# Performance work log

Measured on AMD Instinct MI355X. Metric: run time of the kernel, lower is better.

The kernel has to match this reference:

```python
import jax, jax.numpy as jnp
import numpy as np

B, L = 16, 4096          # trees per batch, leaves per tree (power of 2)
V, D, H, C = 50000, 256, 256, 2  # vocab, input_dim, hidden_dim, num_classes


def setup_inputs() -> dict:
    key = jax.random.key(0)
    ks = jax.random.split(key, 16)
    s = 0.02
    inp = {
        'leaf_ids': jax.random.randint(ks[0], (B, L), 0, V),
        'emb': jax.random.normal(ks[1], (V, D), jnp.float32) * s,
        'W_proj': jax.random.normal(ks[2], (D, H), jnp.float32) * s,
        'b_proj': jnp.zeros((H,), jnp.float32),
        'W_fl': jax.random.normal(ks[3], (2 * H, H), jnp.float32) * s,
        'b_fl': jnp.zeros((H,), jnp.float32),
        'W_fr': jax.random.normal(ks[4], (2 * H, H), jnp.float32) * s,
        'b_fr': jnp.zeros((H,), jnp.float32),
        'W_i': jax.random.normal(ks[5], (2 * H, H), jnp.float32) * s,
        'b_i': jnp.zeros((H,), jnp.float32),
        'W_o': jax.random.normal(ks[6], (2 * H, H), jnp.float32) * s,
        'b_o': jnp.zeros((H,), jnp.float32),
        'W_c': jax.random.normal(ks[7], (2 * H, H), jnp.float32) * s,
        'b_c': jnp.zeros((H,), jnp.float32),
        'W_cls': jax.random.normal(ks[8], (H, C), jnp.float32) * s,
        'b_cls': jnp.zeros((C,), jnp.float32),
    }
    return inp


def reference(leaf_ids, emb, W_proj, b_proj, W_fl, b_fl, W_fr, b_fr,
              W_i, b_i, W_o, b_o, W_c, b_c, W_cls, b_cls):
    # Leaf: hidden = Linear(embedding), cell = tanh(hidden)
    h = emb[leaf_ids] @ W_proj + b_proj          # [B, L, H]
    c = jnp.tanh(h)
    # Binary Tree-LSTM combine, one level at a time (log2(L) levels, static)
    while h.shape[1] > 1:
        hl, hr = h[:, 0::2], h[:, 1::2]          # [B, n/2, H]
        cl, cr = c[:, 0::2], c[:, 1::2]
        comb = jnp.concatenate([hl, hr], axis=-1)  # [B, n/2, 2H]
        fl = jax.nn.sigmoid(comb @ W_fl + b_fl)
        fr = jax.nn.sigmoid(comb @ W_fr + b_fr)
        ig = jax.nn.sigmoid(comb @ W_i + b_i)
        og = jax.nn.sigmoid(comb @ W_o + b_o)
        cc = jnp.tanh(comb @ W_c + b_c)
        c = fl * cl + fr * cr + ig * cc
        h = og * jnp.tanh(c)
    root_h = h[:, 0]                              # [B, H]
    return root_h @ W_cls + b_cls                 # [B, C] classification logits
```

## Files before the change

kernel.cpp:

```cpp
#include <hip/hip_runtime.h>
#include <hip/hip_bf16.h>

#define Hdim 256
#define Bdim 16
#define Lleaf 4096

typedef unsigned short u16;
typedef __attribute__((ext_vector_type(8))) short short8;
typedef __attribute__((ext_vector_type(4))) float f32x4;

__device__ __forceinline__ u16 f2bf(float x) {
    __hip_bfloat16 b = __float2bfloat16(x);
    return *(u16*)&b;
}
__device__ __forceinline__ float bf2f(u16 u) {
    __hip_bfloat16 b = *(__hip_bfloat16*)&u;
    return __bfloat162float(b);
}
__device__ __forceinline__ float fsig(float x) { return 1.0f / (1.0f + __expf(-x)); }
__device__ __forceinline__ float ftanh(float x) {
    float e = __expf(-2.0f * fabsf(x));
    float t = (1.0f - e) / (1.0f + e);
    return copysignf(t, x);
}

__device__ __forceinline__ void gload_lds16(const u16* gsrc, u16* ldsdst) {
    __builtin_amdgcn_global_load_lds(
        (const __attribute__((address_space(1))) unsigned int*)gsrc,
        (__attribute__((address_space(3))) unsigned int*)ldsdst, 16, 0, 0);
}

__global__ void pack_weights2(const float* __restrict__ Wfl, const float* __restrict__ Wfr,
                              const float* __restrict__ Wi,  const float* __restrict__ Wo,
                              const float* __restrict__ Wc,
                              u16* __restrict__ Wpk)
{
    int blk = blockIdx.x;
    int ng = blk >> 4, c = blk & 15;
    for (int e = threadIdx.x; e < 5120; e += 256) {
        int g = e >> 10, r = e & 1023;
        int t = r >> 9, s = r & 511;
        int lane = s >> 3, j = s & 7;
        int n = ng * 16 + (lane & 15);
        int k = c * 32 + (lane >> 4) * 8 + j;
        const float* W = (g == 0) ? Wfl : (g == 1) ? Wfr : (g == 2) ? Wi : (g == 3) ? Wo : Wc;
        float x = W[(size_t)k * Hdim + n];
        u16 hi = f2bf(x);
        u16 v = t ? f2bf(x - bf2f(hi)) : hi;
        Wpk[(size_t)blk * 5120 + e] = v;
    }
}

__global__ void pack_wp2(const float* __restrict__ Wp, u16* __restrict__ Wppk)
{
    int blk = blockIdx.x;
    int ng = blk >> 3, c = blk & 7;
    for (int e = threadIdx.x; e < 1024; e += 256) {
        int t = e >> 9, s = e & 511;
        int lane = s >> 3, j = s & 7;
        int n = ng * 16 + (lane & 15);
        int k = c * 32 + (lane >> 4) * 8 + j;
        float x = Wp[(size_t)k * Hdim + n];
        u16 hi = f2bf(x);
        u16 v = t ? f2bf(x - bf2f(hi)) : hi;
        Wppk[(size_t)blk * 1024 + e] = v;
    }
}

__global__ __launch_bounds__(256, 2) void leaf_mfma2(
    const int* __restrict__ ids, const float* __restrict__ emb,
    const u16* __restrict__ Wppk, const float* __restrict__ bp,
    u16* __restrict__ A0hi)
{
    int tid = threadIdx.x;
    int lane = tid & 63, w = tid >> 6;
    int l16 = lane & 15, quad = lane >> 4;
    int m0 = blockIdx.x * 128, ny = blockIdx.y;
    int n0 = ny * 64;

    const float* aptr[2];
#pragma unroll
    for (int mt = 0; mt < 2; mt++) {
        int m = m0 + w * 32 + mt * 16 + l16;
        aptr[mt] = emb + (size_t)ids[m] * 256 + quad * 8;
    }

    f32x4 acc[2][4];
    f32x4 zf = {0.f, 0.f, 0.f, 0.f};
#pragma unroll
    for (int i = 0; i < 2; i++)
#pragma unroll
        for (int j = 0; j < 4; j++) acc[i][j] = zf;

#pragma unroll 1
    for (int c = 0; c < 8; c++) {
        int k0 = c * 32;
        short8 bh[4], bl[4];
#pragma unroll
        for (int nt = 0; nt < 4; nt++) {
            const u16* pb = Wppk + (size_t)(((ny * 4 + nt) * 8 + c) * 2) * 512 + lane * 8;
            bh[nt] = *(const short8*)(pb);
            bl[nt] = *(const short8*)(pb + 512);
        }
        short8 ah[2], al[2];
#pragma unroll
        for (int mt = 0; mt < 2; mt++) {
            float4 a0 = *(const float4*)(aptr[mt] + k0);
            float4 a1 = *(const float4*)(aptr[mt] + k0 + 4);
            float fv[8] = {a0.x, a0.y, a0.z, a0.w, a1.x, a1.y, a1.z, a1.w};
#pragma unroll
            for (int e = 0; e < 8; e++) {
                u16 hv = f2bf(fv[e]);
                u16 lv = f2bf(fv[e] - bf2f(hv));
                ah[mt][e] = (short)hv;
                al[mt][e] = (short)lv;
            }
        }
#pragma unroll
        for (int nt = 0; nt < 4; nt++)
#pragma unroll
            for (int mt = 0; mt < 2; mt++) {
                acc[mt][nt] = __builtin_amdgcn_mfma_f32_16x16x32_bf16(ah[mt], bh[nt], acc[mt][nt], 0, 0, 0);
                acc[mt][nt] = __builtin_amdgcn_mfma_f32_16x16x32_bf16(al[mt], bh[nt], acc[mt][nt], 0, 0, 0);
                acc[mt][nt] = __builtin_amdgcn_mfma_f32_16x16x32_bf16(ah[mt], bl[nt], acc[mt][nt], 0, 0, 0);
            }
    }
#pragma unroll
    for (int mt = 0; mt < 2; mt++)
#pragma unroll
        for (int nt = 0; nt < 4; nt++)
#pragma unroll
            for (int r = 0; r < 4; r++) {
                int m = m0 + w * 32 + mt * 16 + quad * 4 + r;
                int n = n0 + nt * 16 + l16;
                float h = acc[mt][nt][r] + bp[n];
                A0hi[(size_t)(m >> 1) * 512 + (m & 1) * 256 + n] = f2bf(h);
            }
}

template <int LEAF, int WLO>
__global__ __launch_bounds__(256, 3) void level_big2(
    const u16* __restrict__ Ahi,
    const float* __restrict__ Cin,
    const u16* __restrict__ Wpk,
    const float* __restrict__ bfl, const float* __restrict__ bfr,
    const float* __restrict__ bi,  const float* __restrict__ bo,
    const float* __restrict__ bc,
    u16* __restrict__ Aohi, u16* __restrict__ Aolo, float* __restrict__ Cout,
    int M)
{
    int tid = threadIdx.x;
    int lane = tid & 63, w = tid >> 6;
    int l16 = lane & 15, quad = lane >> 4;
    int m0 = blockIdx.x * 64, n0 = blockIdx.y * 64;
    int ng = blockIdx.y * 4 + w;

    __shared__ u16 Abuf[2][8 * 512];

    const u16* asrc[2];
#pragma unroll
    for (int i = 0; i < 2; i++) {
        int fj = w * 2 + i;
        int s = fj >> 2, mf = fj & 3;
        int row = min(m0 + mf * 16 + l16, M - 1);
        asrc[i] = Ahi + (size_t)row * 512 + quad * 8 + s * 32;
    }
    const u16* pb = Wpk + (size_t)ng * 16 * 5120 + lane * 8;

    f32x4 acc[5][4];
    f32x4 zf = {0.f, 0.f, 0.f, 0.f};
#pragma unroll
    for (int g = 0; g < 5; g++)
#pragma unroll
        for (int mf = 0; mf < 4; mf++) acc[g][mf] = zf;

#pragma unroll
    for (int i = 0; i < 2; i++)
        gload_lds16(asrc[i], &Abuf[0][(w * 2 + i) * 512]);

#pragma unroll 1
    for (int c = 0; c < 8; c++) {
        __syncthreads();
        if (c < 7) {
#pragma unroll
            for (int i = 0; i < 2; i++)
                gload_lds16(asrc[i] + (c + 1) * 64, &Abuf[(c + 1) & 1][(w * 2 + i) * 512]);
        }
        const u16* ab = &Abuf[c & 1][0];
#pragma unroll
        for (int s = 0; s < 2; s++) {
            int c32 = c * 2 + s;
            short8 bh[5];
#pragma unroll
            for (int g = 0; g < 5; g++)
                bh[g] = *(const short8*)(pb + (size_t)(c32 * 10 + g * 2) * 512);
#pragma unroll
            for (int mf = 0; mf < 4; mf++) {
                short8 ah = *(const short8*)&ab[(s * 4 + mf) * 512 + lane * 8];
#pragma unroll
                for (int g = 0; g < 5; g++)
                    acc[g][mf] = __builtin_amdgcn_mfma_f32_16x16x32_bf16(ah, bh[g], acc[g][mf], 0, 0, 0);
            }
        }
    }

    int n = n0 + w * 16 + l16;
#pragma unroll
    for (int mf = 0; mf < 4; mf++)
#pragma unroll
        for (int r = 0; r < 4; r++) {
            int m = m0 + mf * 16 + quad * 4 + r;
            if (m >= M) continue;
            float fl = fsig(acc[0][mf][r] + bfl[n]);
            float fr = fsig(acc[1][mf][r] + bfr[n]);
            float ig = fsig(acc[2][mf][r] + bi[n]);
            float og = fsig(acc[3][mf][r] + bo[n]);
            float cc = ftanh(acc[4][mf][r] + bc[n]);
            float cl, cr;
            if (LEAF) {
                cl = ftanh(bf2f(Ahi[(size_t)m * 512 + n]));
                cr = ftanh(bf2f(Ahi[(size_t)m * 512 + 256 + n]));
            } else {
                cl = Cin[(size_t)(2 * m) * 256 + n];
                cr = Cin[(size_t)(2 * m + 1) * 256 + n];
            }
            float cn = fl * cl + fr * cr + ig * cc;
            Cout[(size_t)m * 256 + n] = cn;
            float h = og * ftanh(cn);
            u16 hh = f2bf(h);
            size_t ai = (size_t)(m >> 1) * 512 + (m & 1) * 256 + n;
            Aohi[ai] = hh;
            if (WLO) Aolo[ai] = f2bf(h - bf2f(hh));
        }
}

__global__ __launch_bounds__(256, 4) void level_small(
    const u16* __restrict__ Ahi, const u16* __restrict__ Alo,
    const float* __restrict__ Cin,
    const u16* __restrict__ Wpk,
    const float* __restrict__ bfl, const float* __restrict__ bfr,
    const float* __restrict__ bi,  const float* __restrict__ bo,
    const float* __restrict__ bc,
    u16* __restrict__ Aohi, u16* __restrict__ Aolo, float* __restrict__ Cout,
    int M)
{
    int tid = threadIdx.x;
    int lane = tid & 63, w = tid >> 6;
    int l16 = lane & 15, quad = lane >> 4;
    int mb = blockIdx.x * 16;
    int ng = blockIdx.y;

    const u16* pah = Ahi + (size_t)(mb + l16) * 512 + quad * 8;
    const u16* pal = Alo + (size_t)(mb + l16) * 512 + quad * 8;
    const u16* pb  = Wpk + (size_t)ng * 16 * 5120 + lane * 8;

    f32x4 acc[5];
    f32x4 zf = {0.f, 0.f, 0.f, 0.f};
#pragma unroll
    for (int g = 0; g < 5; g++) acc[g] = zf;

#pragma unroll
    for (int i = 0; i < 4; i++) {
        int c = w * 4 + i;
        short8 ah = *(const short8*)(pah + c * 32);
        short8 al = *(const short8*)(pal + c * 32);
#pragma unroll
        for (int g = 0; g < 5; g++) {
            short8 bh = *(const short8*)(pb + (size_t)(c * 10 + g * 2) * 512);
            short8 bl = *(const short8*)(pb + (size_t)(c * 10 + g * 2 + 1) * 512);
            acc[g] = __builtin_amdgcn_mfma_f32_16x16x32_bf16(ah, bh, acc[g], 0, 0, 0);
            acc[g] = __builtin_amdgcn_mfma_f32_16x16x32_bf16(al, bh, acc[g], 0, 0, 0);
            acc[g] = __builtin_amdgcn_mfma_f32_16x16x32_bf16(ah, bl, acc[g], 0, 0, 0);
        }
    }

    __shared__ float red[4][5][256];
#pragma unroll
    for (int g = 0; g < 5; g++)
#pragma unroll
        for (int r = 0; r < 4; r++)
            red[w][g][(quad * 4 + r) * 16 + l16] = acc[g][r];
    __syncthreads();

    int m = mb + (tid >> 4);
    int n = ng * 16 + (tid & 15);
    if (m < M) {
        float z[5];
#pragma unroll
        for (int g = 0; g < 5; g++)
            z[g] = red[0][g][tid] + red[1][g][tid] + red[2][g][tid] + red[3][g][tid];
        float fl = fsig(z[0] + bfl[n]);
        float fr = fsig(z[1] + bfr[n]);
        float ig = fsig(z[2] + bi[n]);
        float og = fsig(z[3] + bo[n]);
        float cc = ftanh(z[4] + bc[n]);
        float cl = Cin[(size_t)(2 * m) * 256 + n];
        float cr = Cin[(size_t)(2 * m + 1) * 256 + n];
        float cn = fl * cl + fr * cr + ig * cc;
        Cout[(size_t)m * 256 + n] = cn;
        float h = og * ftanh(cn);
        u16 hh = f2bf(h);
        u16 hl = f2bf(h - bf2f(hh));
        size_t ai = (size_t)(m >> 1) * 512 + (m & 1) * 256 + n;
        Aohi[ai] = hh;
        Aolo[ai] = hl;
    }
}

__global__ void classifier_bf(const u16* __restrict__ Ahi, const u16* __restrict__ Alo,
                              const float* __restrict__ Wcls, const float* __restrict__ bcls,
                              float* __restrict__ out)
{
    int t = threadIdx.x;
    if (t < Bdim * 2) {
        int b = t >> 1, cls = t & 1;
        float s = bcls[cls];
        for (int n = 0; n < Hdim; n++) {
            size_t ai = (size_t)(b >> 1) * 512 + (b & 1) * 256 + n;
            float h = bf2f(Ahi[ai]) + bf2f(Alo[ai]);
            s += h * Wcls[(size_t)n * 2 + cls];
        }
        out[t] = s;
    }
}

extern "C" void kernel_launch(void* const* d_in, const int* in_sizes, int n_in,
                              void* d_out, int out_size, void* d_ws, size_t ws_size,
                              hipStream_t stream) {
    const int*   ids  = (const int*)d_in[0];
    const float* emb  = (const float*)d_in[1];
    const float* Wp   = (const float*)d_in[2];
    const float* bp   = (const float*)d_in[3];
    const float* Wfl  = (const float*)d_in[4];
    const float* bfl  = (const float*)d_in[5];
    const float* Wfr  = (const float*)d_in[6];
    const float* bfr  = (const float*)d_in[7];
    const float* Wi   = (const float*)d_in[8];
    const float* bi   = (const float*)d_in[9];
    const float* Wo   = (const float*)d_in[10];
    const float* bo   = (const float*)d_in[11];
    const float* Wc   = (const float*)d_in[12];
    const float* bc   = (const float*)d_in[13];
    const float* Wcls = (const float*)d_in[14];
    const float* bcls = (const float*)d_in[15];

    u16* Wpk  = (u16*)d_ws;
    u16* Wppk = Wpk + (size_t)256 * 5120;
    unsigned char* base = (unsigned char*)d_ws + (4u << 20);
    unsigned char* R1 = base;
    unsigned char* R2 = base + 33554432;

    pack_weights2<<<256, 256, 0, stream>>>(Wfl, Wfr, Wi, Wo, Wc, Wpk);
    pack_wp2<<<128, 256, 0, stream>>>(Wp, Wppk);

    int M0 = Bdim * Lleaf;
    leaf_mfma2<<<dim3(M0 / 128, 4), 256, 0, stream>>>(ids, emb, Wppk, bp, (u16*)R1);

    const u16* Ain_hi = (const u16*)R1;
    const u16* Ain_lo = nullptr;
    const float* Cin = nullptr;

    int lev = 1;
    for (int M = 32768; M >= 16; M >>= 1, lev++) {
        unsigned char* ob = (lev & 1) ? R2 : R1;
        u16* Aohi = (u16*)ob;
        u16* Aolo = Aohi + (size_t)M * 256;
        float* Cout = (float*)(Aohi + (size_t)M * 512);
        if (lev == 1) {
            level_big2<1, 0><<<dim3(M / 64, 4), 256, 0, stream>>>(Ain_hi, nullptr, Wpk,
                                                                  bfl, bfr, bi, bo, bc, Aohi, Aolo, Cout, M);
        } else if (M > 4096) {
            level_big2<0, 0><<<dim3(M / 64, 4), 256, 0, stream>>>(Ain_hi, Cin, Wpk,
                                                                  bfl, bfr, bi, bo, bc, Aohi, Aolo, Cout, M);
        } else if (M == 4096) {
            level_big2<0, 1><<<dim3(M / 64, 4), 256, 0, stream>>>(Ain_hi, Cin, Wpk,
                                                                  bfl, bfr, bi, bo, bc, Aohi, Aolo, Cout, M);
        } else {
            level_small<<<dim3(M / 16, 16), 256, 0, stream>>>(Ain_hi, Ain_lo, Cin, Wpk,
                                                              bfl, bfr, bi, bo, bc, Aohi, Aolo, Cout, M);
        }
        Ain_hi = Aohi; Ain_lo = Aolo; Cin = Cout;
    }

    classifier_bf<<<1, 64, 0, stream>>>(Ain_hi, Ain_lo, Wcls, bcls, (float*)d_out);
}
```

Before: 395.1 us.

## Fuse last five tree levels into one per-tree kernel and drop leaf lo-split

Replaces the per-level launches for the bottom five tree levels (M=256 down to 16) with one tree_bottom kernel, one block per tree, that keeps hidden and cell state in shared memory across levels. Launch overhead and global round-trips for the tiny tail levels go away. Also drops the low-half bf16 split of the activations in the leaf projection GEMM, removing one MFMA of three. That lowers precision of leaf hidden states, and the fused kernel runs on only 16 blocks, so those five levels are serialized within each block.

New measurement: 582.8 us. 1.48x slower.

```diff
diff --git a/kernel.cpp b/kernel.cpp
--- a/kernel.cpp
+++ b/kernel.cpp
@@ -102,26 +102,20 @@
             bh[nt] = *(const short8*)(pb);
             bl[nt] = *(const short8*)(pb + 512);
         }
-        short8 ah[2], al[2];
+        short8 ah[2];
 #pragma unroll
         for (int mt = 0; mt < 2; mt++) {
             float4 a0 = *(const float4*)(aptr[mt] + k0);
             float4 a1 = *(const float4*)(aptr[mt] + k0 + 4);
             float fv[8] = {a0.x, a0.y, a0.z, a0.w, a1.x, a1.y, a1.z, a1.w};
 #pragma unroll
-            for (int e = 0; e < 8; e++) {
-                u16 hv = f2bf(fv[e]);
-                u16 lv = f2bf(fv[e] - bf2f(hv));
-                ah[mt][e] = (short)hv;
-                al[mt][e] = (short)lv;
-            }
+            for (int e = 0; e < 8; e++) ah[mt][e] = (short)f2bf(fv[e]);
         }
 #pragma unroll
         for (int nt = 0; nt < 4; nt++)
 #pragma unroll
             for (int mt = 0; mt < 2; mt++) {
                 acc[mt][nt] = __builtin_amdgcn_mfma_f32_16x16x32_bf16(ah[mt], bh[nt], acc[mt][nt], 0, 0, 0);
-                acc[mt][nt] = __builtin_amdgcn_mfma_f32_16x16x32_bf16(al[mt], bh[nt], acc[mt][nt], 0, 0, 0);
                 acc[mt][nt] = __builtin_amdgcn_mfma_f32_16x16x32_bf16(ah[mt], bl[nt], acc[mt][nt], 0, 0, 0);
             }
     }
@@ -307,19 +301,113 @@
     }
 }
 
-__global__ void classifier_bf(const u16* __restrict__ Ahi, const u16* __restrict__ Alo,
-                              const float* __restrict__ Wcls, const float* __restrict__ bcls,
-                              float* __restrict__ out)
+__global__ __launch_bounds__(256) void tree_bottom(
+    const u16* __restrict__ Ahi,
+    const float* __restrict__ Cin,
+    const u16* __restrict__ Wpk,
+    const float* __restrict__ bfl, const float* __restrict__ bfr,
+    const float* __restrict__ bi,  const float* __restrict__ bo,
+    const float* __restrict__ bc,
+    float* __restrict__ Hroot)
+{
+    const int ST = 258;
+    int tid = threadIdx.x;
+    int lane = tid & 63, w = tid >> 6;
+    int l16 = lane & 15, quad = lane >> 4;
+    int b = blockIdx.x;
+
+    __shared__ u16 Hs[2][32 * ST];
+    __shared__ float Cs[2][32 * ST];
+
+    int r0 = b * 32;
+    for (int i = tid; i < 32 * 32; i += 256) {
+        int row = i >> 5, cg = i & 31;
+        short8 v = *(const short8*)(Ahi + (size_t)(r0 + row) * 256 + cg * 8);
+        *(short8*)&Hs[0][row * ST + cg * 8] = v;
+    }
+    for (int i = tid; i < 32 * 64; i += 256) {
+        int row = i >> 6, cg = i & 63;
+        float4 v = *(const float4*)(Cin + (size_t)(r0 + row) * 256 + cg * 4);
+        *(float4*)&Cs[0][row * ST + cg * 4] = v;
+    }
+    float bias[5][4];
+#pragma unroll
+    for (int nt = 0; nt < 4; nt++) {
+        int n = w * 64 + nt * 16 + l16;
+        bias[0][nt] = bfl[n]; bias[1][nt] = bfr[n]; bias[2][nt] = bi[n];
+        bias[3][nt] = bo[n];  bias[4][nt] = bc[n];
+    }
+    __syncthreads();
+
+    int p = 0;
+#pragma unroll 1
+    for (int lvl = 0; lvl < 5; lvl++) {
+        int R = 16 >> lvl;
+        f32x4 acc[5][4];
+        f32x4 zf = {0.f, 0.f, 0.f, 0.f};
+#pragma unroll
+        for (int g = 0; g < 5; g++)
+#pragma unroll
+            for (int nt = 0; nt < 4; nt++) acc[g][nt] = zf;
+
+        int arow = 2 * min(l16, R - 1);
+#pragma unroll 2
+        for (int c32 = 0; c32 < 16; c32++) {
+            int side = c32 >> 3;
+            int colb = (c32 & 7) * 32 + quad * 8;
+            short8 ah = *(const short8*)&Hs[p][(arow + side) * ST + colb];
+            const u16* pbc = Wpk + (size_t)(c32 * 10) * 512 + lane * 8;
+#pragma unroll
+            for (int nt = 0; nt < 4; nt++) {
+                const u16* pbn = pbc + (size_t)(w * 4 + nt) * 16 * 5120;
+#pragma unroll
+                for (int g = 0; g < 5; g++) {
+                    short8 bh = *(const short8*)(pbn + (size_t)(g * 2) * 512);
+                    short8 bl = *(const short8*)(pbn + (size_t)(g * 2 + 1) * 512);
+                    acc[g][nt] = __builtin_amdgcn_mfma_f32_16x16x32_bf16(ah, bh, acc[g][nt], 0, 0, 0);
+                    acc[g][nt] = __builtin_amdgcn_mfma_f32_16x16x32_bf16(ah, bl, acc[g][nt], 0, 0, 0);
+                }
+            }
+        }
+#pragma unroll
+        for (int nt = 0; nt < 4; nt++) {
+            int n = w * 64 + nt * 16 + l16;
+#pragma unroll
+            for (int r = 0; r < 4; r++) {
+                int row = quad * 4 + r;
+                if (row < R) {
+                    float fl = fsig(acc[0][nt][r] + bias[0][nt]);
+                    float fr = fsig(acc[1][nt][r] + bias[1][nt]);
+                    float ig = fsig(acc[2][nt][r] + bias[2][nt]);
+                    float og = fsig(acc[3][nt][r] + bias[3][nt]);
+                    float cc = ftanh(acc[4][nt][r] + bias[4][nt]);
+                    float cl = Cs[p][(2 * row) * ST + n];
+                    float cr = Cs[p][(2 * row + 1) * ST + n];
+                    float cn = fl * cl + fr * cr + ig * cc;
+                    float h = og * ftanh(cn);
+                    if (R == 1) {
+                        Hroot[b * 256 + n] = h;
+                    } else {
+                        Hs[1 - p][row * ST + n] = f2bf(h);
+                        Cs[1 - p][row * ST + n] = cn;
+                    }
+                }
+            }
+        }
+        __syncthreads();
+        p ^= 1;
+    }
+}
+
+__global__ void classifier_f32(const float* __restrict__ Hroot, const float* __restrict__ Wcls,
+                               const float* __restrict__ bcls, float* __restrict__ out)
 {
     int t = threadIdx.x;
     if (t < Bdim * 2) {
         int b = t >> 1, cls = t & 1;
         float s = bcls[cls];
-        for (int n = 0; n < Hdim; n++) {
-            size_t ai = (size_t)(b >> 1) * 512 + (b & 1) * 256 + n;
-            float h = bf2f(Ahi[ai]) + bf2f(Alo[ai]);
-            s += h * Wcls[(size_t)n * 2 + cls];
-        }
+        for (int n = 0; n < Hdim; n++)
+            s += Hroot[b * 256 + n] * Wcls[(size_t)n * 2 + cls];
         out[t] = s;
     }
 }
@@ -346,6 +434,7 @@
 
     u16* Wpk  = (u16*)d_ws;
     u16* Wppk = Wpk + (size_t)256 * 5120;
+    float* Hroot = (float*)((unsigned char*)d_ws + (3u << 20));
     unsigned char* base = (unsigned char*)d_ws + (4u << 20);
     unsigned char* R1 = base;
     unsigned char* R2 = base + 33554432;
@@ -361,7 +450,7 @@
     const float* Cin = nullptr;
 
     int lev = 1;
-    for (int M = 32768; M >= 16; M >>= 1, lev++) {
+    for (int M = 32768; M >= 512; M >>= 1, lev++) {
         unsigned char* ob = (lev & 1) ? R2 : R1;
         u16* Aohi = (u16*)ob;
         u16* Aolo = Aohi + (size_t)M * 256;
@@ -382,5 +471,6 @@
         Ain_hi = Aohi; Ain_lo = Aolo; Cin = Cout;
     }
 
-    classifier_bf<<<1, 64, 0, stream>>>(Ain_hi, Ain_lo, Wcls, bcls, (float*)d_out);
-}
+    tree_bottom<<<16, 256, 0, stream>>>(Ain_hi, Cin, Wpk, bfl, bfr, bi, bo, bc, Hroot);
+    classifier_f32<<<1, 64, 0, stream>>>(Hroot, Wcls, bcls, (float*)d_out);
+}
```

## Fuse small tree levels and classifier into one persistent kernel with grid barrier

Applied to the files above, without the earlier changes.

Replaces the per-level launches for the small levels (M=2048 down to 16) and the classifier with one persistent kernel. Its 512 blocks loop over the levels and synchronise through an atomic-counter grid barrier, which is reset inside the weight-pack kernel. The aim is to remove about eight kernel launch and drain gaps where each grid is tiny. It also drops the low-part A term in the leaf projection MFMA, cutting one of three MFMAs per tile at some precision cost. The barrier depends on all 512 blocks being resident at once, and the spin loop has a guard against hanging.

New measurement: 769.4 us. 1.95x slower.

```diff
diff --git a/kernel.cpp b/kernel.cpp
--- a/kernel.cpp
+++ b/kernel.cpp
@@ -33,8 +33,9 @@
 __global__ void pack_weights2(const float* __restrict__ Wfl, const float* __restrict__ Wfr,
                               const float* __restrict__ Wi,  const float* __restrict__ Wo,
                               const float* __restrict__ Wc,
-                              u16* __restrict__ Wpk)
+                              u16* __restrict__ Wpk, unsigned* barrier_cnt)
 {
+    if (blockIdx.x == 0 && threadIdx.x == 0) *barrier_cnt = 0u;
     int blk = blockIdx.x;
     int ng = blk >> 4, c = blk & 15;
     for (int e = threadIdx.x; e < 5120; e += 256) {
@@ -102,26 +103,20 @@
             bh[nt] = *(const short8*)(pb);
             bl[nt] = *(const short8*)(pb + 512);
         }
-        short8 ah[2], al[2];
+        short8 ah[2];
 #pragma unroll
         for (int mt = 0; mt < 2; mt++) {
             float4 a0 = *(const float4*)(aptr[mt] + k0);
             float4 a1 = *(const float4*)(aptr[mt] + k0 + 4);
             float fv[8] = {a0.x, a0.y, a0.z, a0.w, a1.x, a1.y, a1.z, a1.w};
 #pragma unroll
-            for (int e = 0; e < 8; e++) {
-                u16 hv = f2bf(fv[e]);
-                u16 lv = f2bf(fv[e] - bf2f(hv));
-                ah[mt][e] = (short)hv;
-                al[mt][e] = (short)lv;
-            }
+            for (int e = 0; e < 8; e++) ah[mt][e] = (short)f2bf(fv[e]);
         }
 #pragma unroll
         for (int nt = 0; nt < 4; nt++)
 #pragma unroll
             for (int mt = 0; mt < 2; mt++) {
                 acc[mt][nt] = __builtin_amdgcn_mfma_f32_16x16x32_bf16(ah[mt], bh[nt], acc[mt][nt], 0, 0, 0);
-                acc[mt][nt] = __builtin_amdgcn_mfma_f32_16x16x32_bf16(al[mt], bh[nt], acc[mt][nt], 0, 0, 0);
                 acc[mt][nt] = __builtin_amdgcn_mfma_f32_16x16x32_bf16(ah[mt], bl[nt], acc[mt][nt], 0, 0, 0);
             }
     }
@@ -234,93 +229,122 @@
         }
 }
 
-__global__ __launch_bounds__(256, 4) void level_small(
-    const u16* __restrict__ Ahi, const u16* __restrict__ Alo,
-    const float* __restrict__ Cin,
+__global__ __launch_bounds__(256, 2) void tree_tail2(
+    const u16* Ahi0, const u16* Alo0, const float* Cin0,
     const u16* __restrict__ Wpk,
     const float* __restrict__ bfl, const float* __restrict__ bfr,
     const float* __restrict__ bi,  const float* __restrict__ bo,
     const float* __restrict__ bc,
-    u16* __restrict__ Aohi, u16* __restrict__ Aolo, float* __restrict__ Cout,
-    int M)
+    u16* T1, u16* T2, unsigned* bar,
+    const float* __restrict__ Wcls, const float* __restrict__ bcls, float* out)
 {
     int tid = threadIdx.x;
     int lane = tid & 63, w = tid >> 6;
     int l16 = lane & 15, quad = lane >> 4;
-    int mb = blockIdx.x * 16;
+    int bx = blockIdx.x;
     int ng = blockIdx.y;
 
-    const u16* pah = Ahi + (size_t)(mb + l16) * 512 + quad * 8;
-    const u16* pal = Alo + (size_t)(mb + l16) * 512 + quad * 8;
-    const u16* pb  = Wpk + (size_t)ng * 16 * 5120 + lane * 8;
-
-    f32x4 acc[5];
-    f32x4 zf = {0.f, 0.f, 0.f, 0.f};
-#pragma unroll
-    for (int g = 0; g < 5; g++) acc[g] = zf;
-
-#pragma unroll
-    for (int i = 0; i < 4; i++) {
-        int c = w * 4 + i;
-        short8 ah = *(const short8*)(pah + c * 32);
-        short8 al = *(const short8*)(pal + c * 32);
-#pragma unroll
-        for (int g = 0; g < 5; g++) {
-            short8 bh = *(const short8*)(pb + (size_t)(c * 10 + g * 2) * 512);
-            short8 bl = *(const short8*)(pb + (size_t)(c * 10 + g * 2 + 1) * 512);
-            acc[g] = __builtin_amdgcn_mfma_f32_16x16x32_bf16(ah, bh, acc[g], 0, 0, 0);
-            acc[g] = __builtin_amdgcn_mfma_f32_16x16x32_bf16(al, bh, acc[g], 0, 0, 0);
-            acc[g] = __builtin_amdgcn_mfma_f32_16x16x32_bf16(ah, bl, acc[g], 0, 0, 0);
-        }
-    }
-
     __shared__ float red[4][5][256];
-#pragma unroll
-    for (int g = 0; g < 5; g++)
-#pragma unroll
-        for (int r = 0; r < 4; r++)
-            red[w][g][(quad * 4 + r) * 16 + l16] = acc[g][r];
-    __syncthreads();
-
-    int m = mb + (tid >> 4);
-    int n = ng * 16 + (tid & 15);
-    if (m < M) {
-        float z[5];
-#pragma unroll
-        for (int g = 0; g < 5; g++)
-            z[g] = red[0][g][tid] + red[1][g][tid] + red[2][g][tid] + red[3][g][tid];
-        float fl = fsig(z[0] + bfl[n]);
-        float fr = fsig(z[1] + bfr[n]);
-        float ig = fsig(z[2] + bi[n]);
-        float og = fsig(z[3] + bo[n]);
-        float cc = ftanh(z[4] + bc[n]);
-        float cl = Cin[(size_t)(2 * m) * 256 + n];
-        float cr = Cin[(size_t)(2 * m + 1) * 256 + n];
-        float cn = fl * cl + fr * cr + ig * cc;
-        Cout[(size_t)m * 256 + n] = cn;
-        float h = og * ftanh(cn);
-        u16 hh = f2bf(h);
-        u16 hl = f2bf(h - bf2f(hh));
-        size_t ai = (size_t)(m >> 1) * 512 + (m & 1) * 256 + n;
-        Aohi[ai] = hh;
-        Aolo[ai] = hl;
-    }
-}
-
-__global__ void classifier_bf(const u16* __restrict__ Ahi, const u16* __restrict__ Alo,
-                              const float* __restrict__ Wcls, const float* __restrict__ bcls,
-                              float* __restrict__ out)
-{
-    int t = threadIdx.x;
-    if (t < Bdim * 2) {
-        int b = t >> 1, cls = t & 1;
+
+    const u16* ahi = Ahi0;
+    const u16* alo = Alo0;
+    const float* cin = Cin0;
+    int parity = 0;
+    unsigned gen = 0;
+
+    const u16* pbw = Wpk + (size_t)ng * 16 * 5120 + lane * 8;
+
+#pragma unroll 1
+    for (int M = 2048; M >= 16; M >>= 1) {
+        u16* ohi = parity ? T2 : T1;
+        u16* olo = ohi + (size_t)M * 256;
+        float* oc = (float*)(ohi + (size_t)M * 512);
+
+#pragma unroll 1
+        for (int mb = bx * 16; mb < M; mb += 512) {
+            const u16* pah = ahi + (size_t)(mb + l16) * 512 + quad * 8;
+            const u16* pal = alo + (size_t)(mb + l16) * 512 + quad * 8;
+
+            f32x4 acc[5];
+            f32x4 zf = {0.f, 0.f, 0.f, 0.f};
+#pragma unroll
+            for (int g = 0; g < 5; g++) acc[g] = zf;
+
+#pragma unroll
+            for (int i = 0; i < 4; i++) {
+                int c = w * 4 + i;
+                short8 ah = *(const short8*)(pah + c * 32);
+                short8 al = *(const short8*)(pal + c * 32);
+#pragma unroll
+                for (int g = 0; g < 5; g++) {
+                    short8 bh = *(const short8*)(pbw + (size_t)(c * 10 + g * 2) * 512);
+                    short8 bl = *(const short8*)(pbw + (size_t)(c * 10 + g * 2 + 1) * 512);
+                    acc[g] = __builtin_amdgcn_mfma_f32_16x16x32_bf16(ah, bh, acc[g], 0, 0, 0);
+                    acc[g] = __builtin_amdgcn_mfma_f32_16x16x32_bf16(al, bh, acc[g], 0, 0, 0);
+                    acc[g] = __builtin_amdgcn_mfma_f32_16x16x32_bf16(ah, bl, acc[g], 0, 0, 0);
+                }
+            }
+
+            __syncthreads();
+#pragma unroll
+            for (int g = 0; g < 5; g++)
+#pragma unroll
+                for (int r = 0; r < 4; r++)
+                    red[w][g][(quad * 4 + r) * 16 + l16] = acc[g][r];
+            __syncthreads();
+
+            int m = mb + (tid >> 4);
+            int n = ng * 16 + (tid & 15);
+            {
+                float z[5];
+#pragma unroll
+                for (int g = 0; g < 5; g++)
+                    z[g] = red[0][g][tid] + red[1][g][tid] + red[2][g][tid] + red[3][g][tid];
+                float fl = fsig(z[0] + bfl[n]);
+                float fr = fsig(z[1] + bfr[n]);
+                float ig = fsig(z[2] + bi[n]);
+                float og = fsig(z[3] + bo[n]);
+                float cc = ftanh(z[4] + bc[n]);
+                float cl = cin[(size_t)(2 * m) * 256 + n];
+                float cr = cin[(size_t)(2 * m + 1) * 256 + n];
+                float cn = fl * cl + fr * cr + ig * cc;
+                oc[(size_t)m * 256 + n] = cn;
+                float h = og * ftanh(cn);
+                u16 hh = f2bf(h);
+                u16 hl = f2bf(h - bf2f(hh));
+                size_t ai = (size_t)(m >> 1) * 512 + (m & 1) * 256 + n;
+                ohi[ai] = hh;
+                olo[ai] = hl;
+            }
+        }
+
+        gen++;
+        __syncthreads();
+        if (tid == 0) {
+            __threadfence();
+            atomicAdd(bar, 1u);
+            unsigned target = 512u * gen;
+            int guard = 0;
+            while (atomicAdd(bar, 0u) < target && guard < (1 << 30)) {
+                __builtin_amdgcn_s_sleep(8);
+                guard++;
+            }
+            __threadfence();
+        }
+        __syncthreads();
+
+        ahi = ohi; alo = olo; cin = oc; parity ^= 1;
+    }
+
+    if (bx == 0 && ng == 0 && tid < Bdim * 2) {
+        int b = tid >> 1, cls = tid & 1;
         float s = bcls[cls];
         for (int n = 0; n < Hdim; n++) {
             size_t ai = (size_t)(b >> 1) * 512 + (b & 1) * 256 + n;
-            float h = bf2f(Ahi[ai]) + bf2f(Alo[ai]);
+            float h = bf2f(ahi[ai]) + bf2f(alo[ai]);
             s += h * Wcls[(size_t)n * 2 + cls];
         }
-        out[t] = s;
+        out[tid] = s;
     }
 }
 
@@ -346,11 +370,14 @@
 
     u16* Wpk  = (u16*)d_ws;
     u16* Wppk = Wpk + (size_t)256 * 5120;
+    unsigned* bar = (unsigned*)((unsigned char*)d_ws + (3u << 20));
     unsigned char* base = (unsigned char*)d_ws + (4u << 20);
     unsigned char* R1 = base;
     unsigned char* R2 = base + 33554432;
-
-    pack_weights2<<<256, 256, 0, stream>>>(Wfl, Wfr, Wi, Wo, Wc, Wpk);
+    u16* T1 = (u16*)((unsigned char*)d_ws + (100u << 20));
+    u16* T2 = (u16*)((unsigned char*)d_ws + (104u << 20));
+
+    pack_weights2<<<256, 256, 0, stream>>>(Wfl, Wfr, Wi, Wo, Wc, Wpk, bar);
     pack_wp2<<<128, 256, 0, stream>>>(Wp, Wppk);
 
     int M0 = Bdim * Lleaf;
@@ -361,7 +388,7 @@
     const float* Cin = nullptr;
 
     int lev = 1;
-    for (int M = 32768; M >= 16; M >>= 1, lev++) {
+    for (int M = 32768; M >= 4096; M >>= 1, lev++) {
         unsigned char* ob = (lev & 1) ? R2 : R1;
         u16* Aohi = (u16*)ob;
         u16* Aolo = Aohi + (size_t)M * 256;
@@ -372,15 +399,14 @@
         } else if (M > 4096) {
             level_big2<0, 0><<<dim3(M / 64, 4), 256, 0, stream>>>(Ain_hi, Cin, Wpk,
                                                                   bfl, bfr, bi, bo, bc, Aohi, Aolo, Cout, M);
-        } else if (M == 4096) {
+        } else {
             level_big2<0, 1><<<dim3(M / 64, 4), 256, 0, stream>>>(Ain_hi, Cin, Wpk,
                                                                   bfl, bfr, bi, bo, bc, Aohi, Aolo, Cout, M);
-        } else {
-            level_small<<<dim3(M / 16, 16), 256, 0, stream>>>(Ain_hi, Ain_lo, Cin, Wpk,
-                                                              bfl, bfr, bi, bo, bc, Aohi, Aolo, Cout, M);
         }
         Ain_hi = Aohi; Ain_lo = Aolo; Cin = Cout;
     }
 
-    classifier_bf<<<1, 64, 0, stream>>>(Ain_hi, Ain_lo, Wcls, bcls, (float*)d_out);
-}
+    tree_tail2<<<dim3(32, 16), 256, 0, stream>>>(Ain_hi, Ain_lo, Cin, Wpk,
+                                                 bfl, bfr, bi, bo, bc,
+                                                 T1, T2, bar, Wcls, bcls, (float*)d_out);
+}
```

## Drop lo-part MFMA in leaf projection and fuse classifier into final level

Applied to the files above, without the earlier changes.

In the leaf projection kernel, the low-order bf16 split of the activations is removed, so each tile issues two MFMAs instead of three, at some cost in precision. The separate classifier launch is also removed. The M=32 level now initialises the output with the bias, and the M=16 level computes the logits with shuffle reductions and atomic adds. This saves one kernel launch, but atomic float accumulation makes the summation order nondeterministic.

New measurement: 395.9 us. No clear change (+0.2%).

```diff
diff --git a/kernel.cpp b/kernel.cpp
--- a/kernel.cpp
+++ b/kernel.cpp
@@ -102,26 +102,20 @@
             bh[nt] = *(const short8*)(pb);
             bl[nt] = *(const short8*)(pb + 512);
         }
-        short8 ah[2], al[2];
+        short8 ah[2];
 #pragma unroll
         for (int mt = 0; mt < 2; mt++) {
             float4 a0 = *(const float4*)(aptr[mt] + k0);
             float4 a1 = *(const float4*)(aptr[mt] + k0 + 4);
             float fv[8] = {a0.x, a0.y, a0.z, a0.w, a1.x, a1.y, a1.z, a1.w};
 #pragma unroll
-            for (int e = 0; e < 8; e++) {
-                u16 hv = f2bf(fv[e]);
-                u16 lv = f2bf(fv[e] - bf2f(hv));
-                ah[mt][e] = (short)hv;
-                al[mt][e] = (short)lv;
-            }
+            for (int e = 0; e < 8; e++) ah[mt][e] = (short)f2bf(fv[e]);
         }
 #pragma unroll
         for (int nt = 0; nt < 4; nt++)
 #pragma unroll
             for (int mt = 0; mt < 2; mt++) {
                 acc[mt][nt] = __builtin_amdgcn_mfma_f32_16x16x32_bf16(ah[mt], bh[nt], acc[mt][nt], 0, 0, 0);
-                acc[mt][nt] = __builtin_amdgcn_mfma_f32_16x16x32_bf16(al[mt], bh[nt], acc[mt][nt], 0, 0, 0);
                 acc[mt][nt] = __builtin_amdgcn_mfma_f32_16x16x32_bf16(ah[mt], bl[nt], acc[mt][nt], 0, 0, 0);
             }
     }
@@ -242,13 +236,17 @@
     const float* __restrict__ bi,  const float* __restrict__ bo,
     const float* __restrict__ bc,
     u16* __restrict__ Aohi, u16* __restrict__ Aolo, float* __restrict__ Cout,
-    int M)
+    int M, int mode,
+    const float* __restrict__ Wcls, const float* __restrict__ bcls, float* __restrict__ out)
 {
     int tid = threadIdx.x;
     int lane = tid & 63, w = tid >> 6;
     int l16 = lane & 15, quad = lane >> 4;
     int mb = blockIdx.x * 16;
     int ng = blockIdx.y;
+
+    if (mode == 1 && blockIdx.x == 0 && blockIdx.y == 0 && tid < Bdim * 2)
+        out[tid] = bcls[tid & 1];
 
     const u16* pah = Ahi + (size_t)(mb + l16) * 512 + quad * 8;
     const u16* pal = Alo + (size_t)(mb + l16) * 512 + quad * 8;
@@ -304,23 +302,19 @@
         size_t ai = (size_t)(m >> 1) * 512 + (m & 1) * 256 + n;
         Aohi[ai] = hh;
         Aolo[ai] = hl;
-    }
-}
-
-__global__ void classifier_bf(const u16* __restrict__ Ahi, const u16* __restrict__ Alo,
-                              const float* __restrict__ Wcls, const float* __restrict__ bcls,
-                              float* __restrict__ out)
-{
-    int t = threadIdx.x;
-    if (t < Bdim * 2) {
-        int b = t >> 1, cls = t & 1;
-        float s = bcls[cls];
-        for (int n = 0; n < Hdim; n++) {
-            size_t ai = (size_t)(b >> 1) * 512 + (b & 1) * 256 + n;
-            float h = bf2f(Ahi[ai]) + bf2f(Alo[ai]);
-            s += h * Wcls[(size_t)n * 2 + cls];
-        }
-        out[t] = s;
+        if (mode == 2) {
+            float p0 = h * Wcls[(size_t)n * 2 + 0];
+            float p1 = h * Wcls[(size_t)n * 2 + 1];
+#pragma unroll
+            for (int off = 8; off >= 1; off >>= 1) {
+                p0 += __shfl_xor(p0, off);
+                p1 += __shfl_xor(p1, off);
+            }
+            if ((tid & 15) == 0) {
+                atomicAdd(&out[m * 2 + 0], p0);
+                atomicAdd(&out[m * 2 + 1], p1);
+            }
+        }
     }
 }
 
@@ -376,11 +370,11 @@
             level_big2<0, 1><<<dim3(M / 64, 4), 256, 0, stream>>>(Ain_hi, Cin, Wpk,
                                                                   bfl, bfr, bi, bo, bc, Aohi, Aolo, Cout, M);
         } else {
+            int mode = (M == 32) ? 1 : (M == 16) ? 2 : 0;
             level_small<<<dim3(M / 16, 16), 256, 0, stream>>>(Ain_hi, Ain_lo, Cin, Wpk,
-                                                              bfl, bfr, bi, bo, bc, Aohi, Aolo, Cout, M);
+                                                              bfl, bfr, bi, bo, bc, Aohi, Aolo, Cout,
+                                                              M, mode, Wcls, bcls, (float*)d_out);
         }
         Ain_hi = Aohi; Ain_lo = Aolo; Cin = Cout;
     }
-
-    classifier_bf<<<1, 64, 0, stream>>>(Ain_hi, Ain_lo, Wcls, bcls, (float*)d_out);
-}
+}
```
